# Kernel tuning notes

Hardware: AMD Instinct MI355X
Metric: run time of the kernel (lower is better)

## Reference

```python
import jax, jax.numpy as jnp
import numpy as np

H = 12   # num_attention_heads
T = 8    # sample_num (frames)
D = 768  # hidden_size


def ln(x, g, b, eps=1e-12):
    m = x.mean(-1, keepdims=True)
    v = x.var(-1, keepdims=True)
    return (x - m) / jnp.sqrt(v + eps) * g + b


def attn(q, k, v):
    # q: [..., Q, Dh], k/v: [..., K, Dh]
    d = q.shape[-1]
    s = jnp.einsum('...qd,...kd->...qk', q, k) / jnp.sqrt(jnp.asarray(d, q.dtype))
    a = jax.nn.softmax(s, axis=-1)
    return jnp.einsum('...qk,...kd->...qd', a, v)


def mha_divided(x, Wq, bq, Wk, bk, Wv, bv, Wo, bo, mode):
    B, S, Dm = x.shape
    Dh = Dm // H
    P = (S - 1) // T

    def proj(W, b):
        return (x @ W + b).reshape(B, S, H, Dh).transpose(0, 2, 1, 3)  # [B,H,S,Dh]

    q, k, v = proj(Wq, bq), proj(Wk, bk), proj(Wv, bv)

    # cls token attends over the full sequence
    cls_ctx = attn(q[:, :, 0:1], k, v)                       # [B,H,1,Dh]
    cls_out = cls_ctx.transpose(0, 2, 1, 3).reshape(B, 1, Dm) @ Wo + bo

    qp = q[:, :, 1:].reshape(B, H, T, P, Dh)
    kp = k[:, :, 1:].reshape(B, H, T, P, Dh)
    vp = v[:, :, 1:].reshape(B, H, T, P, Dh)
    kc, vc = k[:, :, 0], v[:, :, 0]                          # [B,H,Dh]

    if mode == 'time':
        # each patch attends over [cls] + same patch across T frames
        qt = qp.transpose(0, 1, 3, 2, 4)                     # [B,H,P,T,Dh]
        kt = jnp.concatenate([jnp.broadcast_to(kc[:, :, None, None], (B, H, P, 1, Dh)),
                              kp.transpose(0, 1, 3, 2, 4)], axis=3)  # [B,H,P,T+1,Dh]
        vt = jnp.concatenate([jnp.broadcast_to(vc[:, :, None, None], (B, H, P, 1, Dh)),
                              vp.transpose(0, 1, 3, 2, 4)], axis=3)
        ctx = attn(qt, kt, vt)                               # [B,H,P,T,Dh]
        out = ctx.transpose(0, 3, 2, 1, 4).reshape(B, T * P, Dm)  # [B,T,P,H,Dh]
    else:  # 'space': each frame attends over [cls] + P patches in that frame
        kt = jnp.concatenate([jnp.broadcast_to(kc[:, :, None, None], (B, H, T, 1, Dh)), kp], axis=3)
        vt = jnp.concatenate([jnp.broadcast_to(vc[:, :, None, None], (B, H, T, 1, Dh)), vp], axis=3)
        ctx = attn(qp, kt, vt)                               # [B,H,T,P,Dh]
        out = ctx.transpose(0, 2, 3, 1, 4).reshape(B, T * P, Dm)
    out = out @ Wo + bo
    return jnp.concatenate([cls_out, out], axis=1)


def _forward(hidden_states,
             t_Wq, t_bq, t_Wk, t_bk, t_Wv, t_bv, t_Wo, t_bo,
             s_Wq, s_bq, s_Wk, s_bk, s_Wv, s_bv, s_Wo, s_bo,
             W1, b1, W2, b2,
             ln1_g, ln1_b, ln2_g, ln2_b, ln3_g, ln3_b):
    x = hidden_states
    # divided time attention
    x = x + mha_divided(ln(x, ln1_g, ln1_b), t_Wq, t_bq, t_Wk, t_bk, t_Wv, t_bv, t_Wo, t_bo, 'time')
    # divided space attention
    x = x + mha_divided(ln(x, ln2_g, ln2_b), s_Wq, s_bq, s_Wk, s_bk, s_Wv, s_bv, s_Wo, s_bo, 'space')
    # feed-forward with exact (erf) GELU
    h = ln(x, ln3_g, ln3_b)
    x = x + jax.nn.gelu(h @ W1 + b1, approximate=False) @ W2 + b2
    return x


def setup_inputs() -> dict:
    key = jax.random.key(0)
    ks = jax.random.split(key, 16)

    def w(k, shape, s=0.02):
        return jax.random.normal(k, shape, jnp.float32) * s

    B, S = 8, 1 + T * 196
    inp = {"hidden_states": jax.random.normal(ks[0], (B, S, D), jnp.float32)}
    names = ["t_Wq", "t_Wk", "t_Wv", "t_Wo", "s_Wq", "s_Wk", "s_Wv", "s_Wo"]
    for i, n in enumerate(names):
        inp[n] = w(ks[1 + i], (D, D))
        inp[n.replace("W", "b")] = jnp.zeros((D,), jnp.float32)
    inp["W1"] = w(ks[9], (D, 4 * D)); inp["b1"] = jnp.zeros((4 * D,), jnp.float32)
    inp["W2"] = w(ks[10], (4 * D, D)); inp["b2"] = jnp.zeros((D,), jnp.float32)
    for i in (1, 2, 3):
        inp[f"ln{i}_g"] = jnp.ones((D,), jnp.float32)
        inp[f"ln{i}_b"] = jnp.zeros((D,), jnp.float32)
    return inp


def reference(hidden_states,
              t_Wq, t_bq, t_Wk, t_bk, t_Wv, t_bv, t_Wo, t_bo,
              s_Wq, s_bq, s_Wk, s_bk, s_Wv, s_bv, s_Wo, s_bo,
              W1, b1, W2, b2,
              ln1_g, ln1_b, ln2_g, ln2_b, ln3_g, ln3_b):
    return _forward(hidden_states,
                    t_Wq, t_bq, t_Wk, t_bk, t_Wv, t_bv, t_Wo, t_bo,
                    s_Wq, s_bq, s_Wk, s_bk, s_Wv, s_bv, s_Wo, s_bo,
                    W1, b1, W2, b2,
                    ln1_g, ln1_b, ln2_g, ln2_b, ln3_g, ln3_b)
```

## Files before the change

kernel.cpp:

```cpp
#include <hip/hip_runtime.h>

#define BQ   8
#define SQ   1569
#define BS   12552
#define DM   768
#define NH   12
#define DH   64
#define TT   8
#define PP   196
#define D4   3072
#define QKVN 2304
#define CCH  24
#define CKEY 66

typedef _Float16 f16;
typedef _Float16 f16x8 __attribute__((ext_vector_type(8)));
typedef float    f32x4 __attribute__((ext_vector_type(4)));
typedef unsigned long long u64;

#define Y_OFF    0ULL
#define QKV_OFF  19279872ULL
#define CTX_OFF  77119488ULL
#define H_OFF    19279872ULL
#define W_OFF    96399360ULL

__global__ __launch_bounds__(256) void ln_kernel(const float* __restrict__ x,
                                                 const float* __restrict__ g,
                                                 const float* __restrict__ bta,
                                                 f16* __restrict__ y) {
    int row = blockIdx.x * 4 + (threadIdx.x >> 6);
    int lane = threadIdx.x & 63;
    if (row >= BS) return;
    const float* xr = x + (u64)row * DM;
    float v[12];
    float s = 0.f, s2 = 0.f;
#pragma unroll
    for (int i = 0; i < 12; i++) { v[i] = xr[lane + i * 64]; s += v[i]; s2 += v[i] * v[i]; }
#pragma unroll
    for (int m = 1; m < 64; m <<= 1) { s += __shfl_xor(s, m, 64); s2 += __shfl_xor(s2, m, 64); }
    float mean = s * (1.f / 768.f);
    float var  = s2 * (1.f / 768.f) - mean * mean;
    float rstd = rsqrtf(var + 1e-12f);
    f16* yr = y + (u64)row * DM;
#pragma unroll
    for (int i = 0; i < 12; i++) {
        int c = lane + i * 64;
        yr[c] = (f16)((v[i] - mean) * rstd * g[c] + bta[c]);
    }
}

__global__ __launch_bounds__(256) void transpose_kernel(const float* __restrict__ src,
                                                        f16* __restrict__ dst,
                                                        int R, int C) {
    __shared__ float tile[32][33];
    int bx = blockIdx.x * 32;
    int by = blockIdx.y * 32;
    int tx = threadIdx.x & 31, ty = threadIdx.x >> 5;
#pragma unroll
    for (int i = 0; i < 4; i++) {
        int r = by + ty + i * 8, c = bx + tx;
        if (r < R && c < C) tile[ty + i * 8][tx] = src[(u64)r * C + c];
    }
    __syncthreads();
#pragma unroll
    for (int i = 0; i < 4; i++) {
        int c = bx + ty + i * 8, r = by + tx;
        if (c < C && r < R) dst[(u64)c * R + r] = (f16)tile[tx][ty + i * 8];
    }
}

__global__ __launch_bounds__(256) void bias3_kernel(const float* __restrict__ a,
                                                    const float* __restrict__ b,
                                                    const float* __restrict__ c,
                                                    float* __restrict__ dst) {
    int i = blockIdx.x * 256 + threadIdx.x;
    if (i < 768) { dst[i] = a[i]; dst[i + 768] = b[i]; dst[i + 1536] = c[i]; }
}

template <int NOUT, bool GELU, bool RESID, bool OUTF16>
__global__ __launch_bounds__(256) void gemm_kernel(const f16* __restrict__ A,
                                                   const f16* __restrict__ Bt,
                                                   const float* __restrict__ bias,
                                                   const float* __restrict__ resid,
                                                   float* __restrict__ Cf,
                                                   f16* __restrict__ Ch,
                                                   int K) {
    __shared__ f16 As[128 * 40];
    __shared__ f16 Bs[128 * 40];
    int tid  = threadIdx.x;
    int lane = tid & 63, wave = tid >> 6;
    int wm = wave >> 1, wn = wave & 1;
    int m0 = blockIdx.x * 128, n0 = blockIdx.y * 128;
    int tr = tid >> 2, tc = tid & 3;

    f32x4 acc[4][4];
#pragma unroll
    for (int i = 0; i < 4; i++)
#pragma unroll
        for (int j = 0; j < 4; j++)
#pragma unroll
            for (int r = 0; r < 4; r++) acc[i][j][r] = 0.f;

    for (int k0 = 0; k0 < K; k0 += 32) {
#pragma unroll
        for (int half = 0; half < 2; half++) {
            int r = tr + half * 64;
            int grow = m0 + r;
            uint4 av = make_uint4(0u, 0u, 0u, 0u);
            if (grow < BS) av = *(const uint4*)(A + (u64)grow * K + k0 + tc * 8);
            *(uint4*)(&As[r * 40 + tc * 8]) = av;
            int nrow = n0 + r;
            uint4 bv = *(const uint4*)(Bt + (u64)nrow * K + k0 + tc * 8);
            *(uint4*)(&Bs[r * 40 + tc * 8]) = bv;
        }
        __syncthreads();
        f16x8 af[4], bf[4];
#pragma unroll
        for (int i = 0; i < 4; i++)
            af[i] = *(const f16x8*)(&As[(wm * 64 + i * 16 + (lane & 15)) * 40 + (lane >> 4) * 8]);
#pragma unroll
        for (int j = 0; j < 4; j++)
            bf[j] = *(const f16x8*)(&Bs[(wn * 64 + j * 16 + (lane & 15)) * 40 + (lane >> 4) * 8]);
#pragma unroll
        for (int i = 0; i < 4; i++)
#pragma unroll
            for (int j = 0; j < 4; j++)
                acc[i][j] = __builtin_amdgcn_mfma_f32_16x16x32_f16(af[i], bf[j], acc[i][j], 0, 0, 0);
        __syncthreads();
    }

    int quad = lane >> 4, c0 = lane & 15;
#pragma unroll
    for (int i = 0; i < 4; i++) {
#pragma unroll
        for (int j = 0; j < 4; j++) {
            int col = n0 + wn * 64 + j * 16 + c0;
            float bv = bias[col];
#pragma unroll
            for (int r = 0; r < 4; r++) {
                int row = m0 + wm * 64 + i * 16 + quad * 4 + r;
                if (row < BS) {
                    float v = acc[i][j][r] + bv;
                    if (GELU) v = 0.5f * v * (1.f + erff(v * 0.70710678118654752f));
                    if (RESID) v += resid[(u64)row * NOUT + col];
                    if (OUTF16) Ch[(u64)row * NOUT + col] = (f16)v;
                    else        Cf[(u64)row * NOUT + col] = v;
                }
            }
        }
    }
}

__global__ __launch_bounds__(256) void time_attn_kernel(const f16* __restrict__ qkv,
                                                        f16* __restrict__ ctx) {
    int w = blockIdx.x * 4 + (threadIdx.x >> 6);
    int lane = threadIdx.x & 63;
    int b = w / (NH * PP);
    int rem = w % (NH * PP);
    int h = rem / PP, p = rem % PP;
    u64 bb = (u64)b * SQ;
    int hoff = h * 64 + lane;

    float qv[TT], kv[9], vv[9];
#pragma unroll
    for (int t = 0; t < TT; t++) qv[t] = (float)qkv[(bb + 1 + t * PP + p) * QKVN + hoff];
    kv[0] = (float)qkv[bb * QKVN + 768 + hoff];
    vv[0] = (float)qkv[bb * QKVN + 1536 + hoff];
#pragma unroll
    for (int j = 1; j <= TT; j++) {
        u64 ro = (bb + 1 + (u64)(j - 1) * PP + p) * QKVN;
        kv[j] = (float)qkv[ro + 768 + hoff];
        vv[j] = (float)qkv[ro + 1536 + hoff];
    }
#pragma unroll
    for (int t = 0; t < TT; t++) {
        float s[9];
#pragma unroll
        for (int j = 0; j < 9; j++) {
            float ps = qv[t] * kv[j];
#pragma unroll
            for (int m = 1; m < 64; m <<= 1) ps += __shfl_xor(ps, m, 64);
            s[j] = ps * 0.125f;
        }
        float mx = s[0];
#pragma unroll
        for (int j = 1; j < 9; j++) mx = fmaxf(mx, s[j]);
        float sum = 0.f;
#pragma unroll
        for (int j = 0; j < 9; j++) { s[j] = expf(s[j] - mx); sum += s[j]; }
        float o = 0.f;
#pragma unroll
        for (int j = 0; j < 9; j++) o += s[j] * vv[j];
        o /= sum;
        ctx[(bb + 1 + (u64)t * PP + p) * DM + h * 64 + lane] = (f16)o;
    }
}

__global__ __launch_bounds__(256) void cls_part_kernel(const f16* __restrict__ qkv,
                                                       float* __restrict__ part) {
    int g = blockIdx.x;
    int c = g % CCH, bh = g / CCH;
    int b = bh / NH, h = bh % NH;
    u64 bb = (u64)b * SQ;
    int tid = threadIdx.x, lane = tid & 63, wave = tid >> 6;
    __shared__ float sc[CKEY];
    __shared__ float accbuf[4][64];
    __shared__ float lbuf[4];
    __shared__ float mxs;
    float qd = (float)qkv[bb * QKVN + h * 64 + lane];
    int j0 = c * CKEY;
    int cnt = SQ - j0; if (cnt > CKEY) cnt = CKEY;
    for (int jj = wave; jj < cnt; jj += 4) {
        float p = qd * (float)qkv[(bb + j0 + jj) * QKVN + 768 + h * 64 + lane];
#pragma unroll
        for (int m = 1; m < 64; m <<= 1) p += __shfl_xor(p, m, 64);
        if (lane == 0) sc[jj] = p * 0.125f;
    }
    __syncthreads();
    if (wave == 0) {
        float m = -1e30f;
        for (int j = lane; j < cnt; j += 64) m = fmaxf(m, sc[j]);
#pragma unroll
        for (int s = 1; s < 64; s <<= 1) m = fmaxf(m, __shfl_xor(m, s, 64));
        if (lane == 0) mxs = m;
    }
    __syncthreads();
    float mx = mxs;
    float acc = 0.f, l = 0.f;
    for (int jj = wave; jj < cnt; jj += 4) {
        float w = expf(sc[jj] - mx);
        l += w;
        acc += w * (float)qkv[(bb + j0 + jj) * QKVN + 1536 + h * 64 + lane];
    }
    accbuf[wave][lane] = acc;
    if (lane == 0) lbuf[wave] = l;
    __syncthreads();
    if (tid < 64) {
        float a = accbuf[0][tid] + accbuf[1][tid] + accbuf[2][tid] + accbuf[3][tid];
        float* pb = part + ((u64)bh * CCH + c) * 66;
        if (tid == 0) { pb[0] = mx; pb[1] = lbuf[0] + lbuf[1] + lbuf[2] + lbuf[3]; }
        pb[2 + tid] = a;
    }
}

__global__ __launch_bounds__(256) void cls_comb_kernel(const float* __restrict__ part,
                                                       f16* __restrict__ ctx) {
    int w = blockIdx.x * 4 + (threadIdx.x >> 6);
    int lane = threadIdx.x & 63;
    if (w >= BQ * NH) return;
    int b = w / NH, h = w % NH;
    const float* pb = part + (u64)w * CCH * 66;
    float m = (lane < CCH) ? pb[lane * 66] : -1e30f;
#pragma unroll
    for (int s = 1; s < 64; s <<= 1) m = fmaxf(m, __shfl_xor(m, s, 64));
    float l = (lane < CCH) ? pb[lane * 66 + 1] * expf(pb[lane * 66] - m) : 0.f;
#pragma unroll
    for (int s = 1; s < 64; s <<= 1) l += __shfl_xor(l, s, 64);
    float o = 0.f;
    for (int j = 0; j < CCH; j++) {
        float mj = pb[j * 66];
        o += pb[j * 66 + 2 + lane] * expf(mj - m);
    }
    ctx[((u64)b * SQ) * DM + h * 64 + lane] = (f16)(o / l);
}

__global__ __launch_bounds__(256) void space_attn_kernel(const f16* __restrict__ qkv,
                                                         f16* __restrict__ ctx) {
    int g = blockIdx.x;
    int b = g / (NH * TT);
    int rem = g % (NH * TT);
    int h = rem / TT, t = rem % TT;
    __shared__ __align__(16) f16 Vt[64 * 232];
    __shared__ __align__(16) f16 Ps[4 * 16 * 232];
    u64 bb = (u64)b * SQ;
    int tid = threadIdx.x, lane = tid & 63, wave = tid >> 6;
    int l15 = lane & 15, quad = lane >> 4;

    for (int i = tid; i < 4 * 16 * 232 * 2 / 16; i += 256)
        ((uint4*)Ps)[i] = make_uint4(0u, 0u, 0u, 0u);

    for (int idx = tid; idx < 232 * 8; idx += 256) {
        int c8 = idx / 232;
        int j  = idx - c8 * 232;
        int c  = c8 * 8;
        uint4 vraw = make_uint4(0u, 0u, 0u, 0u);
        if (j < 197) {
            int tok = (j == 0) ? 0 : (1 + t * PP + (j - 1));
            vraw = *(const uint4*)(qkv + (bb + tok) * QKVN + 1536 + h * 64 + c);
        }
        f16x8 vv = *(f16x8*)&vraw;
#pragma unroll
        for (int e = 0; e < 8; e++) Vt[(c + e) * 232 + j] = vv[e];
    }
    __syncthreads();

    f16* myP = Ps + wave * 16 * 232;
    for (int qt = wave; qt < 13; qt += 4) {
        int mloc = qt * 16 + l15;
        int mc = mloc > 195 ? 195 : mloc;
        const f16* qr = qkv + (bb + 1 + (u64)t * PP + mc) * QKVN + h * 64;
        f16x8 qa0 = *(const f16x8*)(qr + quad * 8);
        f16x8 qa1 = *(const f16x8*)(qr + 32 + quad * 8);

        f32x4 s[13];
#pragma unroll
        for (int nt = 0; nt < 13; nt++) { s[nt][0] = 0.f; s[nt][1] = 0.f; s[nt][2] = 0.f; s[nt][3] = 0.f; }
#pragma unroll
        for (int nt = 0; nt < 13; nt++) {
            int n = nt * 16 + l15;
            int ncl = n > 196 ? 196 : n;
            int tok = (ncl == 0) ? 0 : (1 + t * PP + (ncl - 1));
            const f16* kr = qkv + (bb + tok) * QKVN + 768 + h * 64;
            f16x8 kb0 = *(const f16x8*)(kr + quad * 8);
            f16x8 kb1 = *(const f16x8*)(kr + 32 + quad * 8);
            s[nt] = __builtin_amdgcn_mfma_f32_16x16x32_f16(qa0, kb0, s[nt], 0, 0, 0);
            s[nt] = __builtin_amdgcn_mfma_f32_16x16x32_f16(qa1, kb1, s[nt], 0, 0, 0);
        }
        if (l15 >= 5) { s[12][0] = -1e30f; s[12][1] = -1e30f; s[12][2] = -1e30f; s[12][3] = -1e30f; }

        float mx[4] = {-1e30f, -1e30f, -1e30f, -1e30f};
#pragma unroll
        for (int nt = 0; nt < 13; nt++)
#pragma unroll
            for (int r = 0; r < 4; r++) mx[r] = fmaxf(mx[r], s[nt][r]);
#pragma unroll
        for (int m = 1; m < 16; m <<= 1)
#pragma unroll
            for (int r = 0; r < 4; r++) mx[r] = fmaxf(mx[r], __shfl_xor(mx[r], m, 64));

        float sum[4] = {0.f, 0.f, 0.f, 0.f};
#pragma unroll
        for (int nt = 0; nt < 13; nt++)
#pragma unroll
            for (int r = 0; r < 4; r++) {
                float p = exp2f((s[nt][r] - mx[r]) * 0.18033688011112042f);
                s[nt][r] = p;
                sum[r] += p;
            }
#pragma unroll
        for (int m = 1; m < 16; m <<= 1)
#pragma unroll
            for (int r = 0; r < 4; r++) sum[r] += __shfl_xor(sum[r], m, 64);

#pragma unroll
        for (int nt = 0; nt < 13; nt++)
#pragma unroll
            for (int r = 0; r < 4; r++)
                myP[(quad * 4 + r) * 232 + nt * 16 + l15] = (f16)s[nt][r];

        f32x4 o[4];
#pragma unroll
        for (int n2 = 0; n2 < 4; n2++) { o[n2][0] = 0.f; o[n2][1] = 0.f; o[n2][2] = 0.f; o[n2][3] = 0.f; }
#pragma unroll
        for (int kc = 0; kc < 7; kc++) {
            f16x8 pa = *(const f16x8*)(&myP[l15 * 232 + kc * 32 + quad * 8]);
#pragma unroll
            for (int n2 = 0; n2 < 4; n2++) {
                f16x8 vb = *(const f16x8*)(&Vt[(n2 * 16 + l15) * 232 + kc * 32 + quad * 8]);
                o[n2] = __builtin_amdgcn_mfma_f32_16x16x32_f16(pa, vb, o[n2], 0, 0, 0);
            }
        }

        float inv[4];
#pragma unroll
        for (int r = 0; r < 4; r++) inv[r] = 1.f / sum[r];
#pragma unroll
        for (int n2 = 0; n2 < 4; n2++)
#pragma unroll
            for (int r = 0; r < 4; r++) {
                int m = qt * 16 + quad * 4 + r;
                if (m < PP)
                    ctx[(bb + 1 + (u64)t * PP + m) * DM + h * 64 + n2 * 16 + l15] = (f16)(o[n2][r] * inv[r]);
            }
    }
}

extern "C" void kernel_launch(void* const* d_in, const int* in_sizes, int n_in,
                              void* d_out, int out_size, void* d_ws, size_t ws_size,
                              hipStream_t stream) {
    const float* x_in  = (const float*)d_in[0];
    const float* t_Wq  = (const float*)d_in[1];
    const float* t_bq  = (const float*)d_in[2];
    const float* t_Wk  = (const float*)d_in[3];
    const float* t_bk  = (const float*)d_in[4];
    const float* t_Wv  = (const float*)d_in[5];
    const float* t_bv  = (const float*)d_in[6];
    const float* t_Wo  = (const float*)d_in[7];
    const float* t_bo  = (const float*)d_in[8];
    const float* s_Wq  = (const float*)d_in[9];
    const float* s_bq  = (const float*)d_in[10];
    const float* s_Wk  = (const float*)d_in[11];
    const float* s_bk  = (const float*)d_in[12];
    const float* s_Wv  = (const float*)d_in[13];
    const float* s_bv  = (const float*)d_in[14];
    const float* s_Wo  = (const float*)d_in[15];
    const float* s_bo  = (const float*)d_in[16];
    const float* W1    = (const float*)d_in[17];
    const float* b1    = (const float*)d_in[18];
    const float* W2    = (const float*)d_in[19];
    const float* b2    = (const float*)d_in[20];
    const float* ln1g  = (const float*)d_in[21];
    const float* ln1b  = (const float*)d_in[22];
    const float* ln2g  = (const float*)d_in[23];
    const float* ln2b  = (const float*)d_in[24];
    const float* ln3g  = (const float*)d_in[25];
    const float* ln3b  = (const float*)d_in[26];

    char* ws = (char*)d_ws;
    f16* y    = (f16*)(ws + Y_OFF);
    f16* qkv  = (f16*)(ws + QKV_OFF);
    f16* ctx  = (f16*)(ws + CTX_OFF);
    f16* hbuf = (f16*)(ws + H_OFF);
    float* clsP = (float*)(ws + Y_OFF);
    char* wreg = ws + W_OFF;
    f16* tQKV  = (f16*)(wreg);
    f16* tWoT  = (f16*)(wreg + 3538944);
    f16* sQKV  = (f16*)(wreg + 4718592);
    f16* sWoT  = (f16*)(wreg + 8257536);
    f16* W1T   = (f16*)(wreg + 9437184);
    f16* W2T   = (f16*)(wreg + 14155776);
    float* tBias = (float*)(wreg + 18874368);
    float* sBias = (float*)(wreg + 18883584);
    float* xcur  = (float*)d_out;

    dim3 tb(256);
    transpose_kernel<<<dim3(24, 24), tb, 0, stream>>>(t_Wq, tQKV, 768, 768);
    transpose_kernel<<<dim3(24, 24), tb, 0, stream>>>(t_Wk, tQKV + 768 * 768, 768, 768);
    transpose_kernel<<<dim3(24, 24), tb, 0, stream>>>(t_Wv, tQKV + 2 * 768 * 768, 768, 768);
    transpose_kernel<<<dim3(24, 24), tb, 0, stream>>>(t_Wo, tWoT, 768, 768);
    transpose_kernel<<<dim3(24, 24), tb, 0, stream>>>(s_Wq, sQKV, 768, 768);
    transpose_kernel<<<dim3(24, 24), tb, 0, stream>>>(s_Wk, sQKV + 768 * 768, 768, 768);
    transpose_kernel<<<dim3(24, 24), tb, 0, stream>>>(s_Wv, sQKV + 2 * 768 * 768, 768, 768);
    transpose_kernel<<<dim3(24, 24), tb, 0, stream>>>(s_Wo, sWoT, 768, 768);
    transpose_kernel<<<dim3(96, 24), tb, 0, stream>>>(W1, W1T, 768, 3072);
    transpose_kernel<<<dim3(24, 96), tb, 0, stream>>>(W2, W2T, 3072, 768);
    bias3_kernel<<<3, tb, 0, stream>>>(t_bq, t_bk, t_bv, tBias);
    bias3_kernel<<<3, tb, 0, stream>>>(s_bq, s_bk, s_bv, sBias);

    ln_kernel<<<3138, tb, 0, stream>>>(x_in, ln1g, ln1b, y);
    gemm_kernel<QKVN, false, false, true><<<dim3(99, 18), tb, 0, stream>>>(y, tQKV, tBias, nullptr, nullptr, qkv, 768);
    time_attn_kernel<<<4704, tb, 0, stream>>>(qkv, ctx);
    cls_part_kernel<<<BQ * NH * CCH, tb, 0, stream>>>(qkv, clsP);
    cls_comb_kernel<<<24, tb, 0, stream>>>(clsP, ctx);
    gemm_kernel<DM, false, true, false><<<dim3(99, 6), tb, 0, stream>>>(ctx, tWoT, t_bo, x_in, xcur, nullptr, 768);

    ln_kernel<<<3138, tb, 0, stream>>>(xcur, ln2g, ln2b, y);
    gemm_kernel<QKVN, false, false, true><<<dim3(99, 18), tb, 0, stream>>>(y, sQKV, sBias, nullptr, nullptr, qkv, 768);
    space_attn_kernel<<<768, tb, 0, stream>>>(qkv, ctx);
    cls_part_kernel<<<BQ * NH * CCH, tb, 0, stream>>>(qkv, clsP);
    cls_comb_kernel<<<24, tb, 0, stream>>>(clsP, ctx);
    gemm_kernel<DM, false, true, false><<<dim3(99, 6), tb, 0, stream>>>(ctx, sWoT, s_bo, xcur, xcur, nullptr, 768);

    ln_kernel<<<3138, tb, 0, stream>>>(xcur, ln3g, ln3b, y);
    gemm_kernel<D4, true, false, true><<<dim3(99, 24), tb, 0, stream>>>(y, W1T, b1, nullptr, nullptr, hbuf, 768);
    gemm_kernel<DM, false, true, false><<<dim3(99, 6), tb, 0, stream>>>(hbuf, W2T, b2, xcur, xcur, nullptr, 3072);
}
```

Measured before the change: 1.018 ms.

## Load GEMM tiles directly into LDS and remap grid for XCD locality

The GEMM tile loads now use global_load_lds, which copies global data straight into LDS and skips the staging step through VGPRs. The LDS row padding is removed so the wave-contiguous 1 KB write layout that instruction needs lines up. The 2D grid becomes a 1D grid padded to 104 M-blocks so that blocks sharing the same A row-tiles tend to land on the same XCD, which should improve L2 reuse. In exchange, the unpadded LDS rows may cause bank conflicts on fragment reads, and padded blocks exit early; a cosmetic change in cls_part writes the shared max directly.

```diff
diff --git a/kernel.cpp b/kernel.cpp
--- a/kernel.cpp
+++ b/kernel.cpp
@@ -12,11 +12,15 @@
 #define QKVN 2304
 #define CCH  24
 #define CKEY 66
+#define MB_PAD 104
 
 typedef _Float16 f16;
 typedef _Float16 f16x8 __attribute__((ext_vector_type(8)));
 typedef float    f32x4 __attribute__((ext_vector_type(4)));
 typedef unsigned long long u64;
+
+#define AS1 __attribute__((address_space(1)))
+#define AS3 __attribute__((address_space(3)))
 
 #define Y_OFF    0ULL
 #define QKV_OFF  19279872ULL
@@ -85,13 +89,25 @@
                                                    float* __restrict__ Cf,
                                                    f16* __restrict__ Ch,
                                                    int K) {
-    __shared__ f16 As[128 * 40];
-    __shared__ f16 Bs[128 * 40];
+    __shared__ __align__(16) f16 As[128 * 32];
+    __shared__ __align__(16) f16 Bs[128 * 32];
+    int id = blockIdx.x;
+    int mb = id % MB_PAD, nb = id / MB_PAD;
+    if (mb >= 99) return;
     int tid  = threadIdx.x;
     int lane = tid & 63, wave = tid >> 6;
     int wm = wave >> 1, wn = wave & 1;
-    int m0 = blockIdx.x * 128, n0 = blockIdx.y * 128;
-    int tr = tid >> 2, tc = tid & 3;
+    int m0 = mb * 128, n0 = nb * 128;
+
+    int r0   = wave * 16 + (lane >> 2);
+    int coff = (lane & 3) * 8;
+    const f16* ag0 = A + (u64)(m0 + r0) * K + coff;
+    const f16* ag1 = A + (u64)(m0 + r0 + 64) * K + coff;
+    bool av0 = (m0 + r0) < BS, av1 = (m0 + r0 + 64) < BS;
+    const f16* bg0 = Bt + (u64)(n0 + r0) * K + coff;
+    const f16* bg1 = Bt + (u64)(n0 + r0 + 64) * K + coff;
+    AS3 char* asl = (AS3 char*)As + wave * 1024;
+    AS3 char* bsl = (AS3 char*)Bs + wave * 1024;
 
     f32x4 acc[4][4];
 #pragma unroll
@@ -101,26 +117,21 @@
 #pragma unroll
             for (int r = 0; r < 4; r++) acc[i][j][r] = 0.f;
 
+    int l15 = lane & 15, quad = lane >> 4;
     for (int k0 = 0; k0 < K; k0 += 32) {
-#pragma unroll
-        for (int half = 0; half < 2; half++) {
-            int r = tr + half * 64;
-            int grow = m0 + r;
-            uint4 av = make_uint4(0u, 0u, 0u, 0u);
-            if (grow < BS) av = *(const uint4*)(A + (u64)grow * K + k0 + tc * 8);
-            *(uint4*)(&As[r * 40 + tc * 8]) = av;
-            int nrow = n0 + r;
-            uint4 bv = *(const uint4*)(Bt + (u64)nrow * K + k0 + tc * 8);
-            *(uint4*)(&Bs[r * 40 + tc * 8]) = bv;
-        }
+        if (av0) __builtin_amdgcn_global_load_lds((const AS1 void*)ag0, (AS3 void*)asl, 16, 0, 0);
+        if (av1) __builtin_amdgcn_global_load_lds((const AS1 void*)ag1, (AS3 void*)(asl + 4096), 16, 0, 0);
+        __builtin_amdgcn_global_load_lds((const AS1 void*)bg0, (AS3 void*)bsl, 16, 0, 0);
+        __builtin_amdgcn_global_load_lds((const AS1 void*)bg1, (AS3 void*)(bsl + 4096), 16, 0, 0);
+        ag0 += 32; ag1 += 32; bg0 += 32; bg1 += 32;
         __syncthreads();
         f16x8 af[4], bf[4];
 #pragma unroll
         for (int i = 0; i < 4; i++)
-            af[i] = *(const f16x8*)(&As[(wm * 64 + i * 16 + (lane & 15)) * 40 + (lane >> 4) * 8]);
+            af[i] = *(const f16x8*)(&As[(wm * 64 + i * 16 + l15) * 32 + quad * 8]);
 #pragma unroll
         for (int j = 0; j < 4; j++)
-            bf[j] = *(const f16x8*)(&Bs[(wn * 64 + j * 16 + (lane & 15)) * 40 + (lane >> 4) * 8]);
+            bf[j] = *(const f16x8*)(&Bs[(wn * 64 + j * 16 + l15) * 32 + quad * 8]);
 #pragma unroll
         for (int i = 0; i < 4; i++)
 #pragma unroll
@@ -129,7 +140,7 @@
         __syncthreads();
     }
 
-    int quad = lane >> 4, c0 = lane & 15;
+    int c0 = l15;
 #pragma unroll
     for (int i = 0; i < 4; i++) {
 #pragma unroll
@@ -238,7 +249,7 @@
     if (tid < 64) {
         float a = accbuf[0][tid] + accbuf[1][tid] + accbuf[2][tid] + accbuf[3][tid];
         float* pb = part + ((u64)bh * CCH + c) * 66;
-        if (tid == 0) { pb[0] = mx; pb[1] = lbuf[0] + lbuf[1] + lbuf[2] + lbuf[3]; }
+        if (tid == 0) { pb[0] = mxs; pb[1] = lbuf[0] + lbuf[1] + lbuf[2] + lbuf[3]; }
         pb[2 + tid] = a;
     }
 }
@@ -438,20 +449,20 @@
     bias3_kernel<<<3, tb, 0, stream>>>(s_bq, s_bk, s_bv, sBias);
 
     ln_kernel<<<3138, tb, 0, stream>>>(x_in, ln1g, ln1b, y);
-    gemm_kernel<QKVN, false, false, true><<<dim3(99, 18), tb, 0, stream>>>(y, tQKV, tBias, nullptr, nullptr, qkv, 768);
+    gemm_kernel<QKVN, false, false, true><<<MB_PAD * 18, tb, 0, stream>>>(y, tQKV, tBias, nullptr, nullptr, qkv, 768);
     time_attn_kernel<<<4704, tb, 0, stream>>>(qkv, ctx);
     cls_part_kernel<<<BQ * NH * CCH, tb, 0, stream>>>(qkv, clsP);
     cls_comb_kernel<<<24, tb, 0, stream>>>(clsP, ctx);
-    gemm_kernel<DM, false, true, false><<<dim3(99, 6), tb, 0, stream>>>(ctx, tWoT, t_bo, x_in, xcur, nullptr, 768);
+    gemm_kernel<DM, false, true, false><<<MB_PAD * 6, tb, 0, stream>>>(ctx, tWoT, t_bo, x_in, xcur, nullptr, 768);
 
     ln_kernel<<<3138, tb, 0, stream>>>(xcur, ln2g, ln2b, y);
-    gemm_kernel<QKVN, false, false, true><<<dim3(99, 18), tb, 0, stream>>>(y, sQKV, sBias, nullptr, nullptr, qkv, 768);
+    gemm_kernel<QKVN, false, false, true><<<MB_PAD * 18, tb, 0, stream>>>(y, sQKV, sBias, nullptr, nullptr, qkv, 768);
     space_attn_kernel<<<768, tb, 0, stream>>>(qkv, ctx);
     cls_part_kernel<<<BQ * NH * CCH, tb, 0, stream>>>(qkv, clsP);
     cls_comb_kernel<<<24, tb, 0, stream>>>(clsP, ctx);
-    gemm_kernel<DM, false, true, false><<<dim3(99, 6), tb, 0, stream>>>(ctx, sWoT, s_bo, xcur, xcur, nullptr, 768);
+    gemm_kernel<DM, false, true, false><<<MB_PAD * 6, tb, 0, stream>>>(ctx, sWoT, s_bo, xcur, xcur, nullptr, 768);
 
     ln_kernel<<<3138, tb, 0, stream>>>(xcur, ln3g, ln3b, y);
-    gemm_kernel<D4, true, false, true><<<dim3(99, 24), tb, 0, stream>>>(y, W1T, b1, nullptr, nullptr, hbuf, 768);
-    gemm_kernel<DM, false, true, false><<<dim3(99, 6), tb, 0, stream>>>(hbuf, W2T, b2, xcur, xcur, nullptr, 3072);
-}
+    gemm_kernel<D4, true, false, true><<<MB_PAD * 24, tb, 0, stream>>>(y, W1T, b1, nullptr, nullptr, hbuf, 768);
+    gemm_kernel<DM, false, true, false><<<MB_PAD * 6, tb, 0, stream>>>(hbuf, W2T, b2, xcur, xcur, nullptr, 3072);
+}
```

Result: faster. 901.0 us (-11.5%).
